# Optimization experiments

Measured on AMD Instinct MI355X. Metric: run time of the kernel, lower is better.

The kernel has to match this reference:

```python
import jax, jax.numpy as jnp
import numpy as np

NEG_INF = -1e9  # finite large-negative for the additive causal mask
N, H, S, SKV, K, V = 4, 16, 2048, 2048, 128, 128


def setup_inputs() -> dict:
    key = jax.random.key(0)
    k1, k2, k3, k4 = jax.random.split(key, 4)
    seqs = jax.random.normal(k1, (N, H, S, K), dtype=jnp.float32)
    keys = jax.random.normal(k2, (N, H, SKV, K), dtype=jnp.float32)
    values = jax.random.normal(k3, (N, H, SKV, V), dtype=jnp.float32)
    # boolean keep-mask; force first key position valid so no row is fully masked
    kpm = jax.random.randint(k4, (N, SKV), 0, 2) > 0
    kpm = kpm.at[:, 0].set(True)
    # causal additive attention mask, shape (S, S_kv)
    causal = jnp.tril(jnp.ones((S, SKV), dtype=bool))
    attn_mask = jnp.where(causal, 0.0, NEG_INF).astype(jnp.float32)
    return {"seqs": seqs, "keys": keys, "values": values,
            "key_padding_mask": kpm, "attn_mask": attn_mask}


def reference(seqs, keys, values, key_padding_mask, attn_mask):
    # attn_weights: [N,H,S,S_kv]
    scale = seqs.shape[-1] ** -0.5
    w = jnp.einsum('bhsk,bhtk->bhst', seqs, keys) * scale
    w = w + attn_mask  # broadcast (S,S_kv) over (N,H)
    w = jnp.where(key_padding_mask[:, None, None, :], w, -jnp.inf)
    # softmax computed in fp32, then cast back to input dtype (matches torch)
    p = jax.nn.softmax(w.astype(jnp.float32), axis=-1).astype(seqs.dtype)
    attn = jnp.einsum('bhst,bhtv->bhsv', p, values)
    return attn
```

## Files before the change

### kernel.cpp

```cpp
#include <hip/hip_runtime.h>

#define S_Q 2048
#define S_KV 2048
#define D_K 128
#define NH 64
#define QSCALE 0.12751494907890272f

typedef __attribute__((ext_vector_type(8))) short s16x8;
typedef __attribute__((ext_vector_type(16))) float f32x16;

__device__ __attribute__((aligned(16))) unsigned short g_Kb[(size_t)NH * S_KV * D_K];
__device__ __attribute__((aligned(16))) unsigned short g_Vt[(size_t)NH * D_K * S_KV];

__device__ inline unsigned short f2bf(float f) {
  unsigned int u = __float_as_uint(f);
  u += 0x7FFFu + ((u >> 16) & 1u);
  return (unsigned short)(u >> 16);
}

__device__ inline void plane32_swap(unsigned& a, unsigned& b) {
#if __has_builtin(__builtin_amdgcn_permlane32_swap)
  typedef unsigned __attribute__((ext_vector_type(2))) u32x2;
  u32x2 r = __builtin_amdgcn_permlane32_swap(a, b, false, false);
  a = r.x; b = r.y;
#else
  asm volatile("v_permlane32_swap_b32 %0, %1" : "+v"(a), "+v"(b));
#endif
}

__global__ __launch_bounds__(256) void prep_k_kernel(const float* __restrict__ K) {
  size_t g = (size_t)blockIdx.x * 256 + threadIdx.x;
  const float* src = K + g * 8;
  float4 x = *(const float4*)src;
  float4 y = *(const float4*)(src + 4);
  union { uint4 q; unsigned short u[8]; } t;
  t.u[0] = f2bf(x.x); t.u[1] = f2bf(x.y); t.u[2] = f2bf(x.z); t.u[3] = f2bf(x.w);
  t.u[4] = f2bf(y.x); t.u[5] = f2bf(y.y); t.u[6] = f2bf(y.z); t.u[7] = f2bf(y.w);
  ((uint4*)g_Kb)[g] = t.q;
}

__global__ __launch_bounds__(256) void prep_v_kernel(const float* __restrict__ V) {
  __shared__ float tile_f[64][33];
  int bid = blockIdx.x;
  int bh = bid >> 7;
  int rem = bid & 127;
  int t0 = (rem >> 2) << 6;
  int v0 = (rem & 3) << 5;
  int c = threadIdx.x & 31;
  int r8 = threadIdx.x >> 5;
#pragma unroll
  for (int i = 0; i < 8; i++) {
    int r = r8 + i * 8;
    tile_f[r][c] = V[((size_t)(bh * S_KV + t0 + r)) * D_K + v0 + c];
  }
  __syncthreads();
  int vv = threadIdx.x >> 3;
  int jc = threadIdx.x & 7;
  union { uint4 q; unsigned short u[8]; } t;
#pragma unroll
  for (int u8 = 0; u8 < 8; u8++) t.u[u8] = f2bf(tile_f[jc * 8 + u8][vv]);
  *(uint4*)&g_Vt[((size_t)(bh * D_K + v0 + vv)) * S_KV + t0 + jc * 8] = t.q;
}

__global__ __launch_bounds__(256, 2) void attn_kernel(const float* __restrict__ Q,
                                                      const int* __restrict__ kpm,
                                                      float* __restrict__ out) {
  __shared__ unsigned short sK[2][32 * 136];
  __shared__ unsigned short sV[2][128 * 40];
  __shared__ unsigned sMask[64];

  const int bx = blockIdx.x;
  const int bh = ((bx & 7) << 3) | ((bx >> 3) & 7);
  int qp = bx >> 6;
  int qi = (qp & 4) ? ((qp & 8) ? qp - 8 : qp - 4) : ((qp & 8) ? 19 - qp : 15 - qp);
  const int q0 = qi << 7;
  const int tid = threadIdx.x;
  const int w = tid >> 6;
  const int ln = tid & 31;
  const int h = (tid >> 5) & 1;
  const int h8 = h * 8;
  const int qw = q0 + w * 32;
  const int qln = qw + ln;
  const int b = bh >> 4;

  {
    int base = w * 512;
#pragma unroll
    for (int rr = 0; rr < 8; rr++) {
      int idx = base + rr * 64 + (tid & 63);
      unsigned long long bal = __ballot(kpm[b * S_KV + idx] != 0);
      if ((tid & 63) == 0) {
        sMask[(base >> 5) + rr * 2] = (unsigned)bal;
        sMask[(base >> 5) + rr * 2 + 1] = (unsigned)(bal >> 32);
      }
    }
  }

  s16x8 qf[8];
  {
    const float* qrow = Q + ((size_t)(bh * S_Q + qln)) * D_K + h8;
#pragma unroll
    for (int kc = 0; kc < 8; kc++) {
      float4 x = *(const float4*)(qrow + kc * 16);
      float4 y = *(const float4*)(qrow + kc * 16 + 4);
      union { s16x8 v; unsigned short u[8]; } t;
      t.u[0] = f2bf(x.x * QSCALE); t.u[1] = f2bf(x.y * QSCALE);
      t.u[2] = f2bf(x.z * QSCALE); t.u[3] = f2bf(x.w * QSCALE);
      t.u[4] = f2bf(y.x * QSCALE); t.u[5] = f2bf(y.y * QSCALE);
      t.u[6] = f2bf(y.z * QSCALE); t.u[7] = f2bf(y.w * QSCALE);
      qf[kc] = t.v;
    }
  }

  const int id0 = tid, id1 = 256 + tid;
  const int kr0r = id0 >> 4, kr0c = (id0 & 15) * 8;
  const int kr1r = id1 >> 4, kr1c = (id1 & 15) * 8;
  const int vr0r = id0 >> 2, vr0c = (id0 & 3) * 8;
  const int vr1r = id1 >> 2, vr1c = (id1 & 3) * 8;
  uint4 rk0, rk1, rv0, rv1;
  auto load_tile = [&](int t0) {
    rk0 = *(const uint4*)&g_Kb[((size_t)(bh * S_KV + t0 + kr0r)) * D_K + kr0c];
    rk1 = *(const uint4*)&g_Kb[((size_t)(bh * S_KV + t0 + kr1r)) * D_K + kr1c];
    rv0 = *(const uint4*)&g_Vt[((size_t)(bh * D_K + vr0r)) * S_KV + t0 + vr0c];
    rv1 = *(const uint4*)&g_Vt[((size_t)(bh * D_K + vr1r)) * S_KV + t0 + vr1c];
  };
  auto store_tile = [&](int buf) {
    *(uint4*)&sK[buf][kr0r * 136 + kr0c] = rk0;
    *(uint4*)&sK[buf][kr1r * 136 + kr1c] = rk1;
    *(uint4*)&sV[buf][vr0r * 40 + vr0c] = rv0;
    *(uint4*)&sV[buf][vr1r * 40 + vr1c] = rv1;
  };

  f32x16 o[4] = {f32x16{}, f32x16{}, f32x16{}, f32x16{}};
  float lsum = 0.0f;

  const int nT = qi * 4 + 4;
  load_tile(0);
  store_tile(0);
  load_tile(32);
  __syncthreads();

  for (int i = 0; i < nT; i++) {
    const int cur = i & 1;
    if (i + 1 < nT) {
      store_tile(1 - cur);
      if (i + 2 < nT) load_tile((i + 2) * 32);
    }
    const int t0 = i * 32;
    if (t0 <= qw + 31) {
      const unsigned km = sMask[i];
      f32x16 sa = {};
#pragma unroll
      for (int kc = 0; kc < 8; kc++) {
        s16x8 kb = *(const s16x8*)&sK[cur][ln * 136 + kc * 16 + h8];
        sa = __builtin_amdgcn_mfma_f32_32x32x16_bf16(kb, qf[kc], sa, 0, 0, 0);
      }
      int thr = qln - t0;
      unsigned causal = (thr >= 31) ? 0xFFFFFFFFu : ((thr < 0) ? 0u : ((2u << thr) - 1u));
      unsigned pmh = (km & causal) >> (h * 4);
      float p[16];
#pragma unroll
      for (int r = 0; r < 16; r++) {
        const int tb = (r & 3) + 8 * (r >> 2);
        float e = __builtin_amdgcn_exp2f(sa[r]);
        float bitf = (float)((pmh >> tb) & 1u);
        p[r] = e * bitf;
        lsum += p[r];
      }
      unsigned d[8];
#pragma unroll
      for (int m = 0; m < 4; m++) {
        d[2 * m] = __builtin_amdgcn_perm(__float_as_uint(p[4 * m + 1]),
                                         __float_as_uint(p[4 * m + 0]), 0x07060302u);
        d[2 * m + 1] = __builtin_amdgcn_perm(__float_as_uint(p[4 * m + 3]),
                                             __float_as_uint(p[4 * m + 2]), 0x07060302u);
      }
      plane32_swap(d[0], d[2]); plane32_swap(d[1], d[3]);
      plane32_swap(d[4], d[6]); plane32_swap(d[5], d[7]);
      union { unsigned u[4]; s16x8 v; } pu0, pu1;
      pu0.u[0] = d[0]; pu0.u[1] = d[1]; pu0.u[2] = d[2]; pu0.u[3] = d[3];
      pu1.u[0] = d[4]; pu1.u[1] = d[5]; pu1.u[2] = d[6]; pu1.u[3] = d[7];
#pragma unroll
      for (int vt = 0; vt < 4; vt++) {
        s16x8 va = *(const s16x8*)&sV[cur][(vt * 32 + ln) * 40 + h8];
        s16x8 vb = *(const s16x8*)&sV[cur][(vt * 32 + ln) * 40 + 16 + h8];
        o[vt] = __builtin_amdgcn_mfma_f32_32x32x16_bf16(va, pu0.v, o[vt], 0, 0, 0);
        o[vt] = __builtin_amdgcn_mfma_f32_32x32x16_bf16(vb, pu1.v, o[vt], 0, 0, 0);
      }
    }
    __syncthreads();
  }

  float ltot = lsum + __shfl_xor(lsum, 32, 64);
  float invl = 1.0f / ltot;
  size_t orow = ((size_t)(bh * S_Q + qln)) * D_K;
#pragma unroll
  for (int vt = 0; vt < 4; vt++) {
#pragma unroll
    for (int qd = 0; qd < 4; qd++) {
      float4 vv;
      vv.x = o[vt][4 * qd + 0] * invl;
      vv.y = o[vt][4 * qd + 1] * invl;
      vv.z = o[vt][4 * qd + 2] * invl;
      vv.w = o[vt][4 * qd + 3] * invl;
      *(float4*)&out[orow + vt * 32 + qd * 8 + 4 * h] = vv;
    }
  }
}

extern "C" void kernel_launch(void* const* d_in, const int* in_sizes, int n_in,
                              void* d_out, int out_size, void* d_ws, size_t ws_size,
                              hipStream_t stream) {
  const float* Q = (const float*)d_in[0];
  const float* K = (const float*)d_in[1];
  const float* V = (const float*)d_in[2];
  const int* kpm = (const int*)d_in[3];
  float* out = (float*)d_out;
  hipLaunchKernelGGL(prep_k_kernel, dim3(8192), dim3(256), 0, stream, K);
  hipLaunchKernelGGL(prep_v_kernel, dim3(8192), dim3(256), 0, stream, V);
  hipLaunchKernelGGL(attn_kernel, dim3(1024), dim3(256), 0, stream, Q, kpm, out);
}
```

Measured before the change: 323.3 us.

## Fold padding mask into V and compute row sums with MFMA

The key padding mask is applied in the prep stage: masked V rows are zeroed, and a bf16 0/1 mask vector is stored and loaded per tile into LDS. The per-row softmax denominator then comes from an extra MFMA of that mask vector against P, which removes the per-element bit-mask multiply and the scalar lsum accumulation. The causal mask is applied only on the diagonal tile, the P conversion uses the packed cvt_pk_bf16 instruction, s_setprio hints wrap the MFMA sections, and launch bounds ask for 3 blocks per CU. The costs are two extra MFMAs per tile and a global-to-LDS mask load each iteration. The row sum is now taken from bf16-rounded P rather than fp32 P, which slightly changes numerics.

```diff
diff --git a/kernel.cpp b/kernel.cpp
--- a/kernel.cpp
+++ b/kernel.cpp
@@ -4,6 +4,7 @@
 #define S_KV 2048
 #define D_K 128
 #define NH 64
+#define NB 4
 #define QSCALE 0.12751494907890272f
 
 typedef __attribute__((ext_vector_type(8))) short s16x8;
@@ -11,11 +12,18 @@
 
 __device__ __attribute__((aligned(16))) unsigned short g_Kb[(size_t)NH * S_KV * D_K];
 __device__ __attribute__((aligned(16))) unsigned short g_Vt[(size_t)NH * D_K * S_KV];
+__device__ __attribute__((aligned(16))) unsigned short g_kpmf[NB * S_KV];
 
 __device__ inline unsigned short f2bf(float f) {
   unsigned int u = __float_as_uint(f);
   u += 0x7FFFu + ((u >> 16) & 1u);
   return (unsigned short)(u >> 16);
+}
+
+__device__ inline unsigned cvt_pk_bf16(float lo, float hi) {
+  unsigned r;
+  asm("v_cvt_pk_bf16_f32 %0, %1, %2" : "=v"(r) : "v"(lo), "v"(hi));
+  return r;
 }
 
 __device__ inline void plane32_swap(unsigned& a, unsigned& b) {
@@ -28,7 +36,13 @@
 #endif
 }
 
-__global__ __launch_bounds__(256) void prep_k_kernel(const float* __restrict__ K) {
+__device__ inline void gload_lds_4(const void* g, void* l) {
+  __builtin_amdgcn_global_load_lds((const __attribute__((address_space(1))) void*)g,
+                                   (__attribute__((address_space(3))) void*)l, 4, 0, 0);
+}
+
+__global__ __launch_bounds__(256) void prep_k_kernel(const float* __restrict__ K,
+                                                     const int* __restrict__ kpm) {
   size_t g = (size_t)blockIdx.x * 256 + threadIdx.x;
   const float* src = K + g * 8;
   float4 x = *(const float4*)src;
@@ -37,9 +51,12 @@
   t.u[0] = f2bf(x.x); t.u[1] = f2bf(x.y); t.u[2] = f2bf(x.z); t.u[3] = f2bf(x.w);
   t.u[4] = f2bf(y.x); t.u[5] = f2bf(y.y); t.u[6] = f2bf(y.z); t.u[7] = f2bf(y.w);
   ((uint4*)g_Kb)[g] = t.q;
-}
-
-__global__ __launch_bounds__(256) void prep_v_kernel(const float* __restrict__ V) {
+  if (g < (size_t)NB * S_KV)
+    g_kpmf[g] = kpm[g] ? (unsigned short)0x3F80 : (unsigned short)0;
+}
+
+__global__ __launch_bounds__(256) void prep_v_kernel(const float* __restrict__ V,
+                                                     const int* __restrict__ kpm) {
   __shared__ float tile_f[64][33];
   int bid = blockIdx.x;
   int bh = bid >> 7;
@@ -48,10 +65,12 @@
   int v0 = (rem & 3) << 5;
   int c = threadIdx.x & 31;
   int r8 = threadIdx.x >> 5;
+  const int* kp = kpm + (bh >> 4) * S_KV + t0;
 #pragma unroll
   for (int i = 0; i < 8; i++) {
     int r = r8 + i * 8;
-    tile_f[r][c] = V[((size_t)(bh * S_KV + t0 + r)) * D_K + v0 + c];
+    float f = V[((size_t)(bh * S_KV + t0 + r)) * D_K + v0 + c];
+    tile_f[r][c] = kp[r] ? f : 0.0f;
   }
   __syncthreads();
   int vv = threadIdx.x >> 3;
@@ -62,12 +81,11 @@
   *(uint4*)&g_Vt[((size_t)(bh * D_K + v0 + vv)) * S_KV + t0 + jc * 8] = t.q;
 }
 
-__global__ __launch_bounds__(256, 2) void attn_kernel(const float* __restrict__ Q,
-                                                      const int* __restrict__ kpm,
+__global__ __launch_bounds__(256, 3) void attn_kernel(const float* __restrict__ Q,
                                                       float* __restrict__ out) {
-  __shared__ unsigned short sK[2][32 * 136];
-  __shared__ unsigned short sV[2][128 * 40];
-  __shared__ unsigned sMask[64];
+  __shared__ __attribute__((aligned(16))) unsigned short sK[2][32 * 136];
+  __shared__ __attribute__((aligned(16))) unsigned short sV[2][128 * 40];
+  __shared__ __attribute__((aligned(16))) unsigned short sL[2][32];
 
   const int bx = blockIdx.x;
   const int bh = ((bx & 7) << 3) | ((bx >> 3) & 7);
@@ -82,19 +100,7 @@
   const int qw = q0 + w * 32;
   const int qln = qw + ln;
   const int b = bh >> 4;
-
-  {
-    int base = w * 512;
-#pragma unroll
-    for (int rr = 0; rr < 8; rr++) {
-      int idx = base + rr * 64 + (tid & 63);
-      unsigned long long bal = __ballot(kpm[b * S_KV + idx] != 0);
-      if ((tid & 63) == 0) {
-        sMask[(base >> 5) + rr * 2] = (unsigned)bal;
-        sMask[(base >> 5) + rr * 2 + 1] = (unsigned)(bal >> 32);
-      }
-    }
-  }
+  const unsigned short* gkpm = g_kpmf + (size_t)b * S_KV;
 
   s16x8 qf[8];
   {
@@ -132,11 +138,12 @@
   };
 
   f32x16 o[4] = {f32x16{}, f32x16{}, f32x16{}, f32x16{}};
-  float lsum = 0.0f;
+  f32x16 lacc = {};
 
   const int nT = qi * 4 + 4;
   load_tile(0);
   store_tile(0);
+  if (tid < 16) gload_lds_4(gkpm + tid * 2, &sL[0][0]);
   load_tile(32);
   __syncthreads();
 
@@ -144,42 +151,43 @@
     const int cur = i & 1;
     if (i + 1 < nT) {
       store_tile(1 - cur);
+      if (tid < 16) gload_lds_4(gkpm + (i + 1) * 32 + tid * 2, &sL[1 - cur][0]);
       if (i + 2 < nT) load_tile((i + 2) * 32);
     }
     const int t0 = i * 32;
-    if (t0 <= qw + 31) {
-      const unsigned km = sMask[i];
+    if (t0 <= qw) {
       f32x16 sa = {};
+      __builtin_amdgcn_s_setprio(1);
 #pragma unroll
       for (int kc = 0; kc < 8; kc++) {
         s16x8 kb = *(const s16x8*)&sK[cur][ln * 136 + kc * 16 + h8];
         sa = __builtin_amdgcn_mfma_f32_32x32x16_bf16(kb, qf[kc], sa, 0, 0, 0);
       }
-      int thr = qln - t0;
-      unsigned causal = (thr >= 31) ? 0xFFFFFFFFu : ((thr < 0) ? 0u : ((2u << thr) - 1u));
-      unsigned pmh = (km & causal) >> (h * 4);
+      __builtin_amdgcn_s_setprio(0);
       float p[16];
 #pragma unroll
-      for (int r = 0; r < 16; r++) {
-        const int tb = (r & 3) + 8 * (r >> 2);
-        float e = __builtin_amdgcn_exp2f(sa[r]);
-        float bitf = (float)((pmh >> tb) & 1u);
-        p[r] = e * bitf;
-        lsum += p[r];
+      for (int r = 0; r < 16; r++) p[r] = __builtin_amdgcn_exp2f(sa[r]);
+      if (t0 == qw) {
+#pragma unroll
+        for (int r = 0; r < 16; r++) {
+          int tl = (r & 3) + 8 * (r >> 2) + 4 * h;
+          if (tl > ln) p[r] = 0.0f;
+        }
       }
       unsigned d[8];
 #pragma unroll
       for (int m = 0; m < 4; m++) {
-        d[2 * m] = __builtin_amdgcn_perm(__float_as_uint(p[4 * m + 1]),
-                                         __float_as_uint(p[4 * m + 0]), 0x07060302u);
-        d[2 * m + 1] = __builtin_amdgcn_perm(__float_as_uint(p[4 * m + 3]),
-                                             __float_as_uint(p[4 * m + 2]), 0x07060302u);
+        d[2 * m] = cvt_pk_bf16(p[4 * m + 0], p[4 * m + 1]);
+        d[2 * m + 1] = cvt_pk_bf16(p[4 * m + 2], p[4 * m + 3]);
       }
       plane32_swap(d[0], d[2]); plane32_swap(d[1], d[3]);
       plane32_swap(d[4], d[6]); plane32_swap(d[5], d[7]);
       union { unsigned u[4]; s16x8 v; } pu0, pu1;
       pu0.u[0] = d[0]; pu0.u[1] = d[1]; pu0.u[2] = d[2]; pu0.u[3] = d[3];
       pu1.u[0] = d[4]; pu1.u[1] = d[5]; pu1.u[2] = d[6]; pu1.u[3] = d[7];
+      s16x8 lva0 = *(const s16x8*)&sL[cur][h8];
+      s16x8 lva1 = *(const s16x8*)&sL[cur][16 + h8];
+      __builtin_amdgcn_s_setprio(1);
 #pragma unroll
       for (int vt = 0; vt < 4; vt++) {
         s16x8 va = *(const s16x8*)&sV[cur][(vt * 32 + ln) * 40 + h8];
@@ -187,12 +195,14 @@
         o[vt] = __builtin_amdgcn_mfma_f32_32x32x16_bf16(va, pu0.v, o[vt], 0, 0, 0);
         o[vt] = __builtin_amdgcn_mfma_f32_32x32x16_bf16(vb, pu1.v, o[vt], 0, 0, 0);
       }
+      lacc = __builtin_amdgcn_mfma_f32_32x32x16_bf16(lva0, pu0.v, lacc, 0, 0, 0);
+      lacc = __builtin_amdgcn_mfma_f32_32x32x16_bf16(lva1, pu1.v, lacc, 0, 0, 0);
+      __builtin_amdgcn_s_setprio(0);
     }
     __syncthreads();
   }
 
-  float ltot = lsum + __shfl_xor(lsum, 32, 64);
-  float invl = 1.0f / ltot;
+  float invl = 1.0f / lacc[0];
   size_t orow = ((size_t)(bh * S_Q + qln)) * D_K;
 #pragma unroll
   for (int vt = 0; vt < 4; vt++) {
@@ -216,7 +226,7 @@
   const float* V = (const float*)d_in[2];
   const int* kpm = (const int*)d_in[3];
   float* out = (float*)d_out;
-  hipLaunchKernelGGL(prep_k_kernel, dim3(8192), dim3(256), 0, stream, K);
-  hipLaunchKernelGGL(prep_v_kernel, dim3(8192), dim3(256), 0, stream, V);
-  hipLaunchKernelGGL(attn_kernel, dim3(1024), dim3(256), 0, stream, Q, kpm, out);
-}
+  hipLaunchKernelGGL(prep_k_kernel, dim3(8192), dim3(256), 0, stream, K, kpm);
+  hipLaunchKernelGGL(prep_v_kernel, dim3(8192), dim3(256), 0, stream, V, kpm);
+  hipLaunchKernelGGL(attn_kernel, dim3(1024), dim3(256), 0, stream, Q, out);
+}
```

New measurement: 349.4 us. +8.1%, slower.
